# Optimization experiments

Hardware: AMD Instinct MI355X
Metric: run time of the kernel (lower is better)

Reference implementation:

```python
import jax, jax.numpy as jnp
import numpy as np

HIDDEN = 2048
N_HEADS = 32
N_KV = 8
HEAD_DIM = 64
B, S = 2, 2048
EPS = 1e-6
ROT_BASE = 10000.0


def _rms_norm(x, w):
    var = jnp.mean(x * x, axis=-1, keepdims=True)
    return x * jax.lax.rsqrt(var + EPS) * w


def _rotate_half(x):
    h = x.shape[-1] // 2
    return jnp.concatenate([-x[..., h:], x[..., :h]], axis=-1)


def _apply_rope(x, cos, sin):
    # x: [B,S,H,D], cos/sin: [S,D] -> broadcast over batch and heads
    c = cos[None, :, None, :]
    s = sin[None, :, None, :]
    return x * c + _rotate_half(x) * s


def setup_inputs() -> dict:
    key = jax.random.key(0)
    ks = jax.random.split(key, 12)
    sd = 0.02
    hidden_states = jax.random.normal(ks[0], (B, S, HIDDEN), dtype=jnp.float32)
    Wq = jax.random.normal(ks[1], (HIDDEN, N_HEADS * HEAD_DIM), dtype=jnp.float32) * sd
    bq = jnp.zeros((N_HEADS * HEAD_DIM,), dtype=jnp.float32)
    Wk = jax.random.normal(ks[2], (HIDDEN, N_KV * HEAD_DIM), dtype=jnp.float32) * sd
    bk = jnp.zeros((N_KV * HEAD_DIM,), dtype=jnp.float32)
    Wv = jax.random.normal(ks[3], (HIDDEN, N_KV * HEAD_DIM), dtype=jnp.float32) * sd
    bv = jnp.zeros((N_KV * HEAD_DIM,), dtype=jnp.float32)
    Wo = jax.random.normal(ks[4], (N_HEADS * HEAD_DIM, HIDDEN), dtype=jnp.float32) * sd
    bo = jnp.zeros((HIDDEN,), dtype=jnp.float32)
    qn_w = jnp.ones((HEAD_DIM,), dtype=jnp.float32)
    kn_w = jnp.ones((HEAD_DIM,), dtype=jnp.float32)
    # rotary tables (Llama convention: duplicated half-dim freqs)
    inv_freq = 1.0 / (ROT_BASE ** (np.arange(0, HEAD_DIM, 2, dtype=np.float32) / HEAD_DIM))
    t = np.arange(S, dtype=np.float32)
    freqs = np.outer(t, inv_freq)              # [S, D/2]
    emb = np.concatenate([freqs, freqs], axis=-1)  # [S, D]
    cos = jnp.asarray(np.cos(emb), dtype=jnp.float32)
    sin = jnp.asarray(np.sin(emb), dtype=jnp.float32)
    cu_seqlens = jnp.asarray([0, S, 2 * S], dtype=jnp.int32)
    return {"hidden_states": hidden_states, "Wq": Wq, "bq": bq, "Wk": Wk, "bk": bk,
            "Wv": Wv, "bv": bv, "Wo": Wo, "bo": bo, "qn_w": qn_w, "kn_w": kn_w,
            "cos": cos, "sin": sin, "cu_seqlens": cu_seqlens, "max_s": S}


def reference(hidden_states, Wq, bq, Wk, bk, Wv, bv, Wo, bo, qn_w, kn_w, cos, sin, cu_seqlens, max_s):
    b, s, _ = hidden_states.shape
    q = (hidden_states @ Wq + bq).reshape(b, s, N_HEADS, HEAD_DIM)
    k = (hidden_states @ Wk + bk).reshape(b, s, N_KV, HEAD_DIM)
    v = (hidden_states @ Wv + bv).reshape(b, s, N_KV, HEAD_DIM)
    q = _rms_norm(q, qn_w)
    k = _rms_norm(k, kn_w)
    q = _apply_rope(q, cos, sin)
    k = _apply_rope(k, cos, sin)
    # GQA: repeat_interleave kv heads to match query heads
    n_rep = N_HEADS // N_KV
    k = jnp.repeat(k, n_rep, axis=2)
    v = jnp.repeat(v, n_rep, axis=2)
    q = q.transpose(0, 2, 1, 3)  # [B,H,S,D]
    k = k.transpose(0, 2, 1, 3)
    v = v.transpose(0, 2, 1, 3)
    scale = 1.0 / jnp.sqrt(jnp.asarray(HEAD_DIM, dtype=q.dtype))
    scores = jnp.einsum("bhqd,bhkd->bhqk", q, k) * scale
    neg = jnp.finfo(scores.dtype).min
    causal = jnp.triu(jnp.ones((s, s), dtype=scores.dtype), k=1)  # [S,S]
    scores = scores + causal[None, None] * neg
    attn = jax.nn.softmax(scores, axis=-1)
    out = jnp.einsum("bhqk,bhkd->bhqd", attn, v)
    out = out.transpose(0, 2, 1, 3).reshape(b, s, N_HEADS * HEAD_DIM)
    return out @ Wo + bo
```

## Files before the change

### kernel.cpp

```cpp
#include <hip/hip_runtime.h>

typedef unsigned short u16;
typedef __attribute__((ext_vector_type(4))) float f32x4;
typedef __attribute__((ext_vector_type(16))) float f32x16;
typedef __attribute__((ext_vector_type(8))) short s16x8;
typedef __attribute__((ext_vector_type(8))) unsigned short u16x8;
typedef __attribute__((ext_vector_type(4))) unsigned short u16x4;

__device__ __forceinline__ float bf2f(u16 u) {
    union { unsigned int i; float f; } x; x.i = ((unsigned int)u) << 16; return x.f;
}
__device__ __forceinline__ u16 f2bf(float f) {
    union { float f; unsigned int i; } x; x.f = f;
    unsigned int r = x.i + 0x7FFFu + ((x.i >> 16) & 1u);
    return (u16)(r >> 16);
}
__device__ __forceinline__ void gload16(const void* g, void* l) {
    __builtin_amdgcn_global_load_lds((const __attribute__((address_space(1))) void*)g,
                                     (__attribute__((address_space(3))) void*)l, 16, 0, 0);
}
__device__ __forceinline__ unsigned cvtpk(float lo, float hi) {
    unsigned r;
    asm("v_cvt_pk_bf16_f32 %0, %1, %2" : "=v"(r) : "v"(lo), "v"(hi));
    return r;
}

#define BATCH 2
#define SEQ 2048
#define HID 2048
#define NH 32
#define NKV 8
#define HD 64
#define TOK (BATCH * SEQ)
#define NQKV 3072
#define QSCALE 0.18033688011112042f

__global__ void k_f32_to_bf16(const float* __restrict__ src, u16* __restrict__ dst, int n4) {
    int i = blockIdx.x * blockDim.x + threadIdx.x;
    if (i >= n4) return;
    f32x4 v = ((const f32x4*)src)[i];
    u16x4 o;
    o[0] = f2bf(v[0]); o[1] = f2bf(v[1]); o[2] = f2bf(v[2]); o[3] = f2bf(v[3]);
    *(u16x4*)(dst + (size_t)i * 4) = o;
}

__global__ void k_transpose_all(const float* __restrict__ Wq, const float* __restrict__ Wk,
                                const float* __restrict__ Wv, const float* __restrict__ Wo,
                                u16* __restrict__ WTqkv, u16* __restrict__ WoT) {
    __shared__ float tile[32][33];
    const int z = blockIdx.z;
    const float* src;
    u16* dst;
    int N;
    if (z == 0)      { src = Wq; dst = WTqkv;                              N = HID; }
    else if (z == 1) { src = Wk; dst = WTqkv + (size_t)HID * HID;          N = 512; }
    else if (z == 2) { src = Wv; dst = WTqkv + (size_t)(HID + 512) * HID;  N = 512; }
    else             { src = Wo; dst = WoT;                                N = HID; }
    int n0 = blockIdx.x * 32, k0 = blockIdx.y * 32;
    if (n0 >= N) return;
    int tx = threadIdx.x, ty = threadIdx.y;
#pragma unroll
    for (int i = 0; i < 4; i++)
        tile[ty + i * 8][tx] = src[(size_t)(k0 + ty + i * 8) * N + n0 + tx];
    __syncthreads();
#pragma unroll
    for (int i = 0; i < 4; i++) {
        int n = n0 + ty + i * 8;
        dst[(size_t)n * HID + k0 + tx] = f2bf(tile[tx][ty + i * 8]);
    }
}

__global__ void k_transpose_v(const u16* __restrict__ src, u16* __restrict__ dst) {
    __shared__ u16 tile[32][34];
    const u16* s = src + (size_t)blockIdx.z * SEQ * HD;
    u16* d = dst + (size_t)blockIdx.z * SEQ * HD;
    int d0 = blockIdx.x * 32;
    int s0 = blockIdx.y * 32;
    int tx = threadIdx.x, ty = threadIdx.y;
#pragma unroll
    for (int i = 0; i < 4; i++)
        tile[ty + i * 8][tx] = s[(size_t)(s0 + ty + i * 8) * HD + d0 + tx];
    __syncthreads();
#pragma unroll
    for (int i = 0; i < 4; i++)
        d[(size_t)(d0 + ty + i * 8) * SEQ + s0 + tx] = tile[tx][ty + i * 8];
}

__global__ __launch_bounds__(512, 1) void k_gemm256_qkv(const u16* __restrict__ A, const u16* __restrict__ BT,
                                                        const float* __restrict__ bq, const float* __restrict__ bk,
                                                        const float* __restrict__ bv,
                                                        const float* __restrict__ qn_w, const float* __restrict__ kn_w,
                                                        const float* __restrict__ cosT, const float* __restrict__ sinT,
                                                        u16* __restrict__ Qp, u16* __restrict__ Kp, u16* __restrict__ Vp,
                                                        int gxn, int K, int lda, int ldb) {
    __shared__ u16 LDS[2][2][256 * 64];
    const int tid = threadIdx.x;
    const int w = tid >> 6, lane = tid & 63;
    const int wm = w >> 2, wn = w & 3;
    const int lr = lane & 15, g = lane >> 4;
    const int nwg = gridDim.x;
    int bid = blockIdx.x;
    const int cpx = nwg >> 3;
    bid = (bid & 7) * cpx + (bid >> 3);
    const int brow = (bid / gxn) * 256, bcol = (bid % gxn) * 256;

    const int lrow8 = lane >> 3;
    const int gs = (lane & 7) ^ lrow8;
    const u16* Ag[4]; const u16* Bg[4];
#pragma unroll
    for (int p = 0; p < 4; p++) {
        int row = (w * 4 + p) * 8 + lrow8;
        Ag[p] = A + (size_t)(brow + row) * lda + gs * 8;
        Bg[p] = BT + (size_t)(bcol + row) * ldb + gs * 8;
    }

    f32x4 acc[8][4] = {};

#pragma unroll
    for (int p = 0; p < 4; p++) {
        gload16(Ag[p], &LDS[0][0][(w * 4 + p) * 512]);
        gload16(Bg[p], &LDS[0][1][(w * 4 + p) * 512]);
    }
    asm volatile("s_waitcnt vmcnt(0)" ::: "memory");
    __builtin_amdgcn_s_barrier();
    asm volatile("" ::: "memory");

    const int NT = K >> 6;
    int cur = 0;
    for (int tk = 0; tk < NT; tk++) {
        const u16* Al = &LDS[cur][0][0];
        const u16* Bl = &LDS[cur][1][0];
        u16* An = &LDS[cur ^ 1][0][0];
        u16* Bn = &LDS[cur ^ 1][1][0];
        const int knext = (tk + 1) << 6;
        const bool pf = (tk + 1 < NT);
        s16x8 bfr[4][2];
#pragma unroll
        for (int p = 0; p < 4; p++) {
            s16x8 af[2][2];
#pragma unroll
            for (int j = 0; j < 2; j++) {
                const char* rowp = (const char*)Al + (size_t)(wm * 128 + (2 * p + j) * 16 + lr) * 128;
#pragma unroll
                for (int kk = 0; kk < 2; kk++)
                    af[j][kk] = *(const s16x8*)(rowp + (((kk * 4 + g) ^ (lr & 7)) << 4));
            }
            if (p == 0) {
#pragma unroll
                for (int ni = 0; ni < 4; ni++) {
                    const char* rowp = (const char*)Bl + (size_t)(wn * 64 + ni * 16 + lr) * 128;
#pragma unroll
                    for (int kk = 0; kk < 2; kk++)
                        bfr[ni][kk] = *(const s16x8*)(rowp + (((kk * 4 + g) ^ (lr & 7)) << 4));
                }
            }
            if (pf) {
                gload16(Ag[p] + knext, &An[(w * 4 + p) * 512]);
                gload16(Bg[p] + knext, &Bn[(w * 4 + p) * 512]);
            }
            __builtin_amdgcn_s_barrier();
            __builtin_amdgcn_s_setprio(1);
#pragma unroll
            for (int j = 0; j < 2; j++)
#pragma unroll
                for (int ni = 0; ni < 4; ni++) {
                    acc[2 * p + j][ni] = __builtin_amdgcn_mfma_f32_16x16x32_bf16(af[j][0], bfr[ni][0], acc[2 * p + j][ni], 0, 0, 0);
                    acc[2 * p + j][ni] = __builtin_amdgcn_mfma_f32_16x16x32_bf16(af[j][1], bfr[ni][1], acc[2 * p + j][ni], 0, 0, 0);
                }
            __builtin_amdgcn_s_setprio(0);
            __builtin_amdgcn_s_barrier();
        }
        if (pf) asm volatile("s_waitcnt vmcnt(0)" ::: "memory");
        __builtin_amdgcn_s_barrier();
        asm volatile("" ::: "memory");
        cur ^= 1;
    }

    const int head = (bcol >> 6) + wn;
    const float* bptr = (head < 32) ? (bq + head * 64)
                       : (head < 40) ? (bk + (head - 32) * 64)
                                     : (bv + (head - 40) * 64);
    const float bz0 = bptr[0 * 16 + lr], bz1 = bptr[1 * 16 + lr];
    const float bz2 = bptr[2 * 16 + lr], bz3 = bptr[3 * 16 + lr];
    const float nw0 = (head < 32) ? qn_w[0 * 16 + lr] : kn_w[0 * 16 + lr];
    const float nw1 = (head < 32) ? qn_w[1 * 16 + lr] : kn_w[1 * 16 + lr];
    const float nw2 = (head < 32) ? qn_w[2 * 16 + lr] : kn_w[2 * 16 + lr];
    const float nw3 = (head < 32) ? qn_w[3 * 16 + lr] : kn_w[3 * 16 + lr];
#pragma unroll
    for (int mi = 0; mi < 8; mi++) {
#pragma unroll
        for (int r = 0; r < 4; r++) {
            int row = brow + wm * 128 + mi * 16 + g * 4 + r;
            int b = row >> 11, s = row & 2047;
            float v[4];
            v[0] = acc[mi][0][r] + bz0;
            v[1] = acc[mi][1][r] + bz1;
            v[2] = acc[mi][2][r] + bz2;
            v[3] = acc[mi][3][r] + bz3;
            if (head < 40) {
                float ss = v[0] * v[0] + v[1] * v[1] + v[2] * v[2] + v[3] * v[3];
                ss += __shfl_xor(ss, 1);
                ss += __shfl_xor(ss, 2);
                ss += __shfl_xor(ss, 4);
                ss += __shfl_xor(ss, 8);
                float rin = rsqrtf(ss * (1.0f / 64.0f) + 1e-6f);
                float xn[4];
                xn[0] = v[0] * rin * nw0;
                xn[1] = v[1] * rin * nw1;
                xn[2] = v[2] * rin * nw2;
                xn[3] = v[3] * rin * nw3;
                const float* cr = cosT + (size_t)s * HD;
                const float* sr = sinT + (size_t)s * HD;
                float o[4];
#pragma unroll
                for (int ni = 0; ni < 4; ni++) {
                    int d = ni * 16 + lr;
                    float part = xn[ni ^ 2];
                    float sign = (d < 32) ? -1.f : 1.f;
                    o[ni] = xn[ni] * cr[d] + sign * part * sr[d];
                }
                if (head < 32) {
                    u16* qrow = Qp + (((size_t)(b * NH + head) * SEQ + s) * HD);
#pragma unroll
                    for (int ni = 0; ni < 4; ni++) qrow[ni * 16 + lr] = f2bf(o[ni] * QSCALE);
                } else {
                    u16* krow = Kp + (((size_t)(b * NKV + head - 32) * SEQ + s) * HD);
#pragma unroll
                    for (int ni = 0; ni < 4; ni++) krow[ni * 16 + lr] = f2bf(o[ni]);
                }
            } else {
                u16* vrow = Vp + (((size_t)(b * NKV + head - 40) * SEQ + s) * HD);
#pragma unroll
                for (int ni = 0; ni < 4; ni++) vrow[ni * 16 + lr] = f2bf(v[ni]);
            }
        }
    }
}

__global__ __launch_bounds__(512, 1) void k_gemm_wo(const u16* __restrict__ A, const u16* __restrict__ BT,
                                                    const float* __restrict__ bias, float* __restrict__ Cout,
                                                    int gxn, int K, int lda, int ldb, int N) {
    __shared__ u16 LA[2][128 * 64];
    __shared__ u16 LB[2][256 * 64];
    const int tid = threadIdx.x;
    const int w = tid >> 6, lane = tid & 63;
    const int wm = w >> 2, wn = w & 3;
    const int lr = lane & 15, g = lane >> 4;
    const int nwg = gridDim.x;
    int bid = blockIdx.x;
    const int cpx = nwg >> 3;
    bid = (bid & 7) * cpx + (bid >> 3);
    const int brow = (bid / gxn) * 128, bcol = (bid % gxn) * 256;

    const int lrow8 = lane >> 3;
    const int gs = (lane & 7) ^ lrow8;
    const u16* Ag[2]; const u16* Bg[4];
#pragma unroll
    for (int p = 0; p < 2; p++) {
        int row = (w * 2 + p) * 8 + lrow8;
        Ag[p] = A + (size_t)(brow + row) * lda + gs * 8;
    }
#pragma unroll
    for (int p = 0; p < 4; p++) {
        int row = (w * 4 + p) * 8 + lrow8;
        Bg[p] = BT + (size_t)(bcol + row) * ldb + gs * 8;
    }

    f32x4 acc[4][4] = {};

#pragma unroll
    for (int p = 0; p < 2; p++) gload16(Ag[p], &LA[0][(w * 2 + p) * 512]);
#pragma unroll
    for (int p = 0; p < 4; p++) gload16(Bg[p], &LB[0][(w * 4 + p) * 512]);
    asm volatile("s_waitcnt vmcnt(0)" ::: "memory");
    __builtin_amdgcn_s_barrier();
    asm volatile("" ::: "memory");

    const int NT = K >> 6;
    int cur = 0;
    for (int tk = 0; tk < NT; tk++) {
        const u16* Al = &LA[cur][0];
        const u16* Bl = &LB[cur][0];
        u16* An = &LA[cur ^ 1][0];
        u16* Bn = &LB[cur ^ 1][0];
        const int knext = (tk + 1) << 6;
        const bool pf = (tk + 1 < NT);
        s16x8 bfr[4][2];
#pragma unroll
        for (int p = 0; p < 4; p++) {
            s16x8 af[2];
            const char* rowpA = (const char*)Al + (size_t)(wm * 64 + p * 16 + lr) * 128;
#pragma unroll
            for (int kk = 0; kk < 2; kk++)
                af[kk] = *(const s16x8*)(rowpA + (((kk * 4 + g) ^ (lr & 7)) << 4));
            if (p == 0) {
#pragma unroll
                for (int ni = 0; ni < 4; ni++) {
                    const char* rowp = (const char*)Bl + (size_t)(wn * 64 + ni * 16 + lr) * 128;
#pragma unroll
                    for (int kk = 0; kk < 2; kk++)
                        bfr[ni][kk] = *(const s16x8*)(rowp + (((kk * 4 + g) ^ (lr & 7)) << 4));
                }
            }
            if (pf) {
                if (p == 0) {
                    gload16(Ag[0] + knext, &An[(w * 2 + 0) * 512]);
                    gload16(Ag[1] + knext, &An[(w * 2 + 1) * 512]);
                } else if (p == 1) {
                    gload16(Bg[0] + knext, &Bn[(w * 4 + 0) * 512]);
                    gload16(Bg[1] + knext, &Bn[(w * 4 + 1) * 512]);
                } else if (p == 2) {
                    gload16(Bg[2] + knext, &Bn[(w * 4 + 2) * 512]);
                    gload16(Bg[3] + knext, &Bn[(w * 4 + 3) * 512]);
                }
            }
            __builtin_amdgcn_s_barrier();
            __builtin_amdgcn_s_setprio(1);
#pragma unroll
            for (int ni = 0; ni < 4; ni++) {
                acc[p][ni] = __builtin_amdgcn_mfma_f32_16x16x32_bf16(af[0], bfr[ni][0], acc[p][ni], 0, 0, 0);
                acc[p][ni] = __builtin_amdgcn_mfma_f32_16x16x32_bf16(af[1], bfr[ni][1], acc[p][ni], 0, 0, 0);
            }
            __builtin_amdgcn_s_setprio(0);
            __builtin_amdgcn_s_barrier();
        }
        if (pf) asm volatile("s_waitcnt vmcnt(0)" ::: "memory");
        __builtin_amdgcn_s_barrier();
        asm volatile("" ::: "memory");
        cur ^= 1;
    }

#pragma unroll
    for (int mi = 0; mi < 4; mi++) {
#pragma unroll
        for (int ni = 0; ni < 4; ni++) {
#pragma unroll
            for (int r = 0; r < 4; r++) {
                int row = brow + wm * 64 + mi * 16 + g * 4 + r;
                int col = bcol + wn * 64 + ni * 16 + lr;
                Cout[(size_t)row * N + col] = acc[mi][ni][r] + bias[col];
            }
        }
    }
}

__global__ __launch_bounds__(256) void k_attn_mfma(const u16* __restrict__ Qp, const u16* __restrict__ Kp,
                                                   const u16* __restrict__ VpT, u16* __restrict__ AO) {
    __shared__ u16 K_lds[64 * 64];
    __shared__ u16 VT_lds[64 * 64];
    __shared__ u16 P_lds[4][32][76];
    const int bid = blockIdx.x;
    const int qt = 15 - (bid >> 6);
    const int hh = bid & 63;
    const int b = hh >> 5, h = hh & 31, kvh = h >> 2;
    const int t = threadIdx.x, w = t >> 6, lane = t & 63;
    const int q5 = lane & 31, hi = lane >> 5;
    const int qwb = qt * 128 + w * 32;
    const int q_abs = qwb + q5;

    const u16* Qb = Qp + (size_t)(b * NH + h) * SEQ * HD;
    const u16* Kb = Kp + (size_t)(b * NKV + kvh) * SEQ * HD;
    const u16* Vb = VpT + (size_t)(b * NKV + kvh) * HD * SEQ;

    s16x8 qf0 = *(const s16x8*)(Qb + (size_t)q_abs * HD + 0 * 16 + hi * 8);
    s16x8 qf1 = *(const s16x8*)(Qb + (size_t)q_abs * HD + 1 * 16 + hi * 8);
    s16x8 qf2 = *(const s16x8*)(Qb + (size_t)q_abs * HD + 2 * 16 + hi * 8);
    s16x8 qf3 = *(const s16x8*)(Qb + (size_t)q_abs * HD + 3 * 16 + hi * 8);

    f32x16 O0, O1;
#pragma unroll
    for (int r = 0; r < 16; r++) { O0[r] = 0.f; O1[r] = 0.f; }
    float m = -1e30f, l = 0.f;

    const int swz = (q5 & 7) << 4;
    const int nkt = 2 * (qt + 1);
    for (int kt = 0; kt < nkt; kt++) {
        const int k0 = kt * 64;
        __syncthreads();
#pragma unroll
        for (int i = 0; i < 2; i++) {
            int c = (w * 2 + i) * 64 + lane;
            int row = c >> 3, gslot = (c & 7) ^ (row & 7);
            gload16(Kb + (size_t)(k0 + row) * HD + gslot * 8, (char*)K_lds + (size_t)(w * 2 + i) * 1024);
            gload16(Vb + (size_t)row * SEQ + k0 + gslot * 8, (char*)VT_lds + (size_t)(w * 2 + i) * 1024);
        }
        __syncthreads();
        if (k0 > qwb + 31) continue;

        f32x16 s0, s1;
#pragma unroll
        for (int r = 0; r < 16; r++) { s0[r] = 0.f; s1[r] = 0.f; }
        __builtin_amdgcn_s_setprio(1);
#pragma unroll
        for (int dblk = 0; dblk < 4; dblk++) {
            s16x8 kf0 = *(const s16x8*)((const char*)K_lds + q5 * 128 + ((dblk * 32 + hi * 16) ^ swz));
            s16x8 kf1 = *(const s16x8*)((const char*)K_lds + (32 + q5) * 128 + ((dblk * 32 + hi * 16) ^ swz));
            s16x8 qq = (dblk == 0) ? qf0 : (dblk == 1) ? qf1 : (dblk == 2) ? qf2 : qf3;
            s0 = __builtin_amdgcn_mfma_f32_32x32x16_bf16(kf0, qq, s0, 0, 0, 0);
            s1 = __builtin_amdgcn_mfma_f32_32x32x16_bf16(kf1, qq, s1, 0, 0, 0);
        }
        __builtin_amdgcn_s_setprio(0);

        if (k0 + 63 > qwb) {
            const int qrel = q_abs - k0;
#pragma unroll
            for (int r = 0; r < 16; r++) {
                int kr = (r & 3) + 8 * (r >> 2) + 4 * hi;
                if (kr > qrel) s0[r] = -1e30f;
                if (kr + 32 > qrel) s1[r] = -1e30f;
            }
        }

        float mt = -1e30f;
#pragma unroll
        for (int r = 0; r < 16; r++) { mt = fmaxf(mt, s0[r]); mt = fmaxf(mt, s1[r]); }
        mt = fmaxf(mt, __shfl_xor(mt, 32));
        if (!__all(mt <= m + 8.0f)) {
            float mn = fmaxf(m, mt);
            float f = exp2f(m - mn);
            l *= f;
#pragma unroll
            for (int r = 0; r < 16; r++) { O0[r] *= f; O1[r] *= f; }
            m = mn;
        }
        float ps = 0.f;
#pragma unroll
        for (int r = 0; r < 16; r++) {
            float p0 = exp2f(s0[r] - m);
            float p1 = exp2f(s1[r] - m);
            s0[r] = p0; s1[r] = p1;
            ps += p0 + p1;
        }
        ps += __shfl_xor(ps, 32);
        l += ps;

#pragma unroll
        for (int i = 0; i < 8; i++) {
            int key = 2 * (i & 1) + 8 * (i >> 1) + 4 * hi;
            *(unsigned*)&P_lds[w][q5][key]      = cvtpk(s0[2 * i], s0[2 * i + 1]);
            *(unsigned*)&P_lds[w][q5][key + 32] = cvtpk(s1[2 * i], s1[2 * i + 1]);
        }

        __builtin_amdgcn_s_setprio(1);
#pragma unroll
        for (int ks = 0; ks < 4; ks++) {
            s16x8 pb  = *(const s16x8*)&P_lds[w][q5][ks * 16 + hi * 8];
            s16x8 vf0 = *(const s16x8*)((const char*)VT_lds + q5 * 128 + ((ks * 32 + hi * 16) ^ swz));
            s16x8 vf1 = *(const s16x8*)((const char*)VT_lds + (32 + q5) * 128 + ((ks * 32 + hi * 16) ^ swz));
            O0 = __builtin_amdgcn_mfma_f32_32x32x16_bf16(vf0, pb, O0, 0, 0, 0);
            O1 = __builtin_amdgcn_mfma_f32_32x32x16_bf16(vf1, pb, O1, 0, 0, 0);
        }
        __builtin_amdgcn_s_setprio(0);
    }

    float inv = 1.0f / l;
    u16* orow = AO + (size_t)(b * SEQ + q_abs) * (NH * HD) + h * HD;
#pragma unroll
    for (int db = 0; db < 2; db++) {
#pragma unroll
        for (int g2 = 0; g2 < 4; g2++) {
            u16x4 wv;
#pragma unroll
            for (int i2 = 0; i2 < 4; i2++) {
                float v = (db == 0 ? O0[g2 * 4 + i2] : O1[g2 * 4 + i2]) * inv;
                wv[i2] = f2bf(v);
            }
            *(u16x4*)(orow + db * 32 + g2 * 8 + hi * 4) = wv;
        }
    }
}

extern "C" void kernel_launch(void* const* d_in, const int* in_sizes, int n_in,
                              void* d_out, int out_size, void* d_ws, size_t ws_size,
                              hipStream_t stream) {
    const float* hs   = (const float*)d_in[0];
    const float* Wq   = (const float*)d_in[1];
    const float* bq   = (const float*)d_in[2];
    const float* Wk   = (const float*)d_in[3];
    const float* bk   = (const float*)d_in[4];
    const float* Wv   = (const float*)d_in[5];
    const float* bv   = (const float*)d_in[6];
    const float* Wo   = (const float*)d_in[7];
    const float* bo   = (const float*)d_in[8];
    const float* qn_w = (const float*)d_in[9];
    const float* kn_w = (const float*)d_in[10];
    const float* cosT = (const float*)d_in[11];
    const float* sinT = (const float*)d_in[12];

    char* ws = (char*)d_ws;
    size_t off = 0;
    auto alloc = [&](size_t bytes) { char* p = ws + off; off = (off + bytes + 255) & ~(size_t)255; return p; };
    u16*   Xb    = (u16*)  alloc((size_t)TOK * HID * 2);
    u16*   WTqkv = (u16*)  alloc((size_t)NQKV * HID * 2);
    u16*   WoT   = (u16*)  alloc((size_t)HID * HID * 2);
    u16*   Qp    = (u16*)  alloc((size_t)BATCH * NH * SEQ * HD * 2);
    u16*   Kp    = (u16*)  alloc((size_t)BATCH * NKV * SEQ * HD * 2);
    u16*   Vp    = (u16*)  alloc((size_t)BATCH * NKV * SEQ * HD * 2);
    u16*   VpT   = (u16*)  alloc((size_t)BATCH * NKV * SEQ * HD * 2);
    u16*   AO    = (u16*)  alloc((size_t)TOK * HID * 2);
    (void)ws_size;

    k_f32_to_bf16<<<(TOK * HID / 4 + 255) / 256, 256, 0, stream>>>(hs, Xb, TOK * HID / 4);
    dim3 tb(32, 8);
    k_transpose_all<<<dim3(64, 64, 4), tb, 0, stream>>>(Wq, Wk, Wv, Wo, WTqkv, WoT);
    k_gemm256_qkv<<<dim3((TOK / 256) * (NQKV / 256)), 512, 0, stream>>>(
        Xb, WTqkv, bq, bk, bv, qn_w, kn_w, cosT, sinT, Qp, Kp, Vp, NQKV / 256, HID, HID, HID);
    k_transpose_v<<<dim3(HD / 32, SEQ / 32, BATCH * NKV), tb, 0, stream>>>(Vp, VpT);
    k_attn_mfma<<<BATCH * NH * (SEQ / 128), 256, 0, stream>>>(Qp, Kp, VpT, AO);
    k_gemm_wo<<<dim3((TOK / 128) * (HID / 256)), 512, 0, stream>>>(AO, WoT, bo, (float*)d_out,
                                                                    HID / 256, HID, HID, HID, HID);
}
```

Baseline: 229.3 us.

## Double-buffer K/V tiles in attention kernel to overlap loads with compute

Doubles the LDS buffers for K and V^T and prefetches the next 64-key tile via global_load_lds while the current tile is consumed. Explicit vmcnt waits and s_barrier replace the two __syncthreads per iteration, so the global-to-LDS latency can be hidden behind the MFMA and softmax work. This doubles the K/V LDS footprint, which may reduce occupancy. It also relies on hand-placed waitcnt and barriers being correct.

```diff
diff --git a/kernel.cpp b/kernel.cpp
--- a/kernel.cpp
+++ b/kernel.cpp
@@ -346,8 +346,8 @@
 
 __global__ __launch_bounds__(256) void k_attn_mfma(const u16* __restrict__ Qp, const u16* __restrict__ Kp,
                                                    const u16* __restrict__ VpT, u16* __restrict__ AO) {
-    __shared__ u16 K_lds[64 * 64];
-    __shared__ u16 VT_lds[64 * 64];
+    __shared__ u16 K_lds[2][64 * 64];
+    __shared__ u16 VT_lds[2][64 * 64];
     __shared__ u16 P_lds[4][32][76];
     const int bid = blockIdx.x;
     const int qt = 15 - (bid >> 6);
@@ -362,6 +362,10 @@
     const u16* Kb = Kp + (size_t)(b * NKV + kvh) * SEQ * HD;
     const u16* Vb = VpT + (size_t)(b * NKV + kvh) * HD * SEQ;
 
+    const int c0 = (w * 2 + 0) * 64 + lane, c1 = (w * 2 + 1) * 64 + lane;
+    const int r0 = c0 >> 3, g0 = (c0 & 7) ^ (r0 & 7);
+    const int r1 = c1 >> 3, g1 = (c1 & 7) ^ (r1 & 7);
+
     s16x8 qf0 = *(const s16x8*)(Qb + (size_t)q_abs * HD + 0 * 16 + hi * 8);
     s16x8 qf1 = *(const s16x8*)(Qb + (size_t)q_abs * HD + 1 * 16 + hi * 8);
     s16x8 qf2 = *(const s16x8*)(Qb + (size_t)q_abs * HD + 2 * 16 + hi * 8);
@@ -374,83 +378,103 @@
 
     const int swz = (q5 & 7) << 4;
     const int nkt = 2 * (qt + 1);
+
+    gload16(Kb + (size_t)r0 * HD + g0 * 8, (char*)K_lds[0] + (size_t)(w * 2 + 0) * 1024);
+    gload16(Kb + (size_t)r1 * HD + g1 * 8, (char*)K_lds[0] + (size_t)(w * 2 + 1) * 1024);
+    gload16(Vb + (size_t)r0 * SEQ + g0 * 8, (char*)VT_lds[0] + (size_t)(w * 2 + 0) * 1024);
+    gload16(Vb + (size_t)r1 * SEQ + g1 * 8, (char*)VT_lds[0] + (size_t)(w * 2 + 1) * 1024);
+    asm volatile("s_waitcnt vmcnt(0)" ::: "memory");
+    __builtin_amdgcn_s_barrier();
+    asm volatile("" ::: "memory");
+
     for (int kt = 0; kt < nkt; kt++) {
         const int k0 = kt * 64;
-        __syncthreads();
-#pragma unroll
-        for (int i = 0; i < 2; i++) {
-            int c = (w * 2 + i) * 64 + lane;
-            int row = c >> 3, gslot = (c & 7) ^ (row & 7);
-            gload16(Kb + (size_t)(k0 + row) * HD + gslot * 8, (char*)K_lds + (size_t)(w * 2 + i) * 1024);
-            gload16(Vb + (size_t)row * SEQ + k0 + gslot * 8, (char*)VT_lds + (size_t)(w * 2 + i) * 1024);
-        }
-        __syncthreads();
-        if (k0 > qwb + 31) continue;
-
-        f32x16 s0, s1;
-#pragma unroll
-        for (int r = 0; r < 16; r++) { s0[r] = 0.f; s1[r] = 0.f; }
-        __builtin_amdgcn_s_setprio(1);
-#pragma unroll
-        for (int dblk = 0; dblk < 4; dblk++) {
-            s16x8 kf0 = *(const s16x8*)((const char*)K_lds + q5 * 128 + ((dblk * 32 + hi * 16) ^ swz));
-            s16x8 kf1 = *(const s16x8*)((const char*)K_lds + (32 + q5) * 128 + ((dblk * 32 + hi * 16) ^ swz));
-            s16x8 qq = (dblk == 0) ? qf0 : (dblk == 1) ? qf1 : (dblk == 2) ? qf2 : qf3;
-            s0 = __builtin_amdgcn_mfma_f32_32x32x16_bf16(kf0, qq, s0, 0, 0, 0);
-            s1 = __builtin_amdgcn_mfma_f32_32x32x16_bf16(kf1, qq, s1, 0, 0, 0);
-        }
-        __builtin_amdgcn_s_setprio(0);
-
-        if (k0 + 63 > qwb) {
-            const int qrel = q_abs - k0;
+        const int cur = kt & 1;
+        if (kt + 1 < nkt) {
+            const int nk0 = k0 + 64;
+            gload16(Kb + (size_t)(nk0 + r0) * HD + g0 * 8, (char*)K_lds[cur ^ 1] + (size_t)(w * 2 + 0) * 1024);
+            gload16(Kb + (size_t)(nk0 + r1) * HD + g1 * 8, (char*)K_lds[cur ^ 1] + (size_t)(w * 2 + 1) * 1024);
+            gload16(Vb + (size_t)r0 * SEQ + nk0 + g0 * 8, (char*)VT_lds[cur ^ 1] + (size_t)(w * 2 + 0) * 1024);
+            gload16(Vb + (size_t)r1 * SEQ + nk0 + g1 * 8, (char*)VT_lds[cur ^ 1] + (size_t)(w * 2 + 1) * 1024);
+            asm volatile("s_waitcnt vmcnt(4)" ::: "memory");
+        } else {
+            asm volatile("s_waitcnt vmcnt(0)" ::: "memory");
+        }
+        __builtin_amdgcn_s_barrier();
+        asm volatile("" ::: "memory");
+
+        if (k0 <= qwb + 31) {
+            const char* Kc = (const char*)K_lds[cur];
+            const char* Vc = (const char*)VT_lds[cur];
+
+            f32x16 s0, s1;
+#pragma unroll
+            for (int r = 0; r < 16; r++) { s0[r] = 0.f; s1[r] = 0.f; }
+            __builtin_amdgcn_s_setprio(1);
+#pragma unroll
+            for (int dblk = 0; dblk < 4; dblk++) {
+                s16x8 kf0 = *(const s16x8*)(Kc + q5 * 128 + ((dblk * 32 + hi * 16) ^ swz));
+                s16x8 kf1 = *(const s16x8*)(Kc + (32 + q5) * 128 + ((dblk * 32 + hi * 16) ^ swz));
+                s16x8 qq = (dblk == 0) ? qf0 : (dblk == 1) ? qf1 : (dblk == 2) ? qf2 : qf3;
+                s0 = __builtin_amdgcn_mfma_f32_32x32x16_bf16(kf0, qq, s0, 0, 0, 0);
+                s1 = __builtin_amdgcn_mfma_f32_32x32x16_bf16(kf1, qq, s1, 0, 0, 0);
+            }
+            __builtin_amdgcn_s_setprio(0);
+
+            if (k0 + 63 > qwb) {
+                const int qrel = q_abs - k0;
+#pragma unroll
+                for (int r = 0; r < 16; r++) {
+                    int kr = (r & 3) + 8 * (r >> 2) + 4 * hi;
+                    if (kr > qrel) s0[r] = -1e30f;
+                    if (kr + 32 > qrel) s1[r] = -1e30f;
+                }
+            }
+
+            float mt = -1e30f;
+#pragma unroll
+            for (int r = 0; r < 16; r++) { mt = fmaxf(mt, s0[r]); mt = fmaxf(mt, s1[r]); }
+            mt = fmaxf(mt, __shfl_xor(mt, 32));
+            if (!__all(mt <= m + 8.0f)) {
+                float mn = fmaxf(m, mt);
+                float f = exp2f(m - mn);
+                l *= f;
+#pragma unroll
+                for (int r = 0; r < 16; r++) { O0[r] *= f; O1[r] *= f; }
+                m = mn;
+            }
+            float ps = 0.f;
 #pragma unroll
             for (int r = 0; r < 16; r++) {
-                int kr = (r & 3) + 8 * (r >> 2) + 4 * hi;
-                if (kr > qrel) s0[r] = -1e30f;
-                if (kr + 32 > qrel) s1[r] = -1e30f;
-            }
-        }
-
-        float mt = -1e30f;
-#pragma unroll
-        for (int r = 0; r < 16; r++) { mt = fmaxf(mt, s0[r]); mt = fmaxf(mt, s1[r]); }
-        mt = fmaxf(mt, __shfl_xor(mt, 32));
-        if (!__all(mt <= m + 8.0f)) {
-            float mn = fmaxf(m, mt);
-            float f = exp2f(m - mn);
-            l *= f;
-#pragma unroll
-            for (int r = 0; r < 16; r++) { O0[r] *= f; O1[r] *= f; }
-            m = mn;
-        }
-        float ps = 0.f;
-#pragma unroll
-        for (int r = 0; r < 16; r++) {
-            float p0 = exp2f(s0[r] - m);
-            float p1 = exp2f(s1[r] - m);
-            s0[r] = p0; s1[r] = p1;
-            ps += p0 + p1;
-        }
-        ps += __shfl_xor(ps, 32);
-        l += ps;
-
-#pragma unroll
-        for (int i = 0; i < 8; i++) {
-            int key = 2 * (i & 1) + 8 * (i >> 1) + 4 * hi;
-            *(unsigned*)&P_lds[w][q5][key]      = cvtpk(s0[2 * i], s0[2 * i + 1]);
-            *(unsigned*)&P_lds[w][q5][key + 32] = cvtpk(s1[2 * i], s1[2 * i + 1]);
-        }
-
-        __builtin_amdgcn_s_setprio(1);
-#pragma unroll
-        for (int ks = 0; ks < 4; ks++) {
-            s16x8 pb  = *(const s16x8*)&P_lds[w][q5][ks * 16 + hi * 8];
-            s16x8 vf0 = *(const s16x8*)((const char*)VT_lds + q5 * 128 + ((ks * 32 + hi * 16) ^ swz));
-            s16x8 vf1 = *(const s16x8*)((const char*)VT_lds + (32 + q5) * 128 + ((ks * 32 + hi * 16) ^ swz));
-            O0 = __builtin_amdgcn_mfma_f32_32x32x16_bf16(vf0, pb, O0, 0, 0, 0);
-            O1 = __builtin_amdgcn_mfma_f32_32x32x16_bf16(vf1, pb, O1, 0, 0, 0);
-        }
-        __builtin_amdgcn_s_setprio(0);
+                float p0 = exp2f(s0[r] - m);
+                float p1 = exp2f(s1[r] - m);
+                s0[r] = p0; s1[r] = p1;
+                ps += p0 + p1;
+            }
+            ps += __shfl_xor(ps, 32);
+            l += ps;
+
+#pragma unroll
+            for (int i = 0; i < 8; i++) {
+                int key = 2 * (i & 1) + 8 * (i >> 1) + 4 * hi;
+                *(unsigned*)&P_lds[w][q5][key]      = cvtpk(s0[2 * i], s0[2 * i + 1]);
+                *(unsigned*)&P_lds[w][q5][key + 32] = cvtpk(s1[2 * i], s1[2 * i + 1]);
+            }
+
+            __builtin_amdgcn_s_setprio(1);
+#pragma unroll
+            for (int ks = 0; ks < 4; ks++) {
+                s16x8 pb  = *(const s16x8*)&P_lds[w][q5][ks * 16 + hi * 8];
+                s16x8 vf0 = *(const s16x8*)(Vc + q5 * 128 + ((ks * 32 + hi * 16) ^ swz));
+                s16x8 vf1 = *(const s16x8*)(Vc + (32 + q5) * 128 + ((ks * 32 + hi * 16) ^ swz));
+                O0 = __builtin_amdgcn_mfma_f32_32x32x16_bf16(vf0, pb, O0, 0, 0, 0);
+                O1 = __builtin_amdgcn_mfma_f32_32x32x16_bf16(vf1, pb, O1, 0, 0, 0);
+            }
+            __builtin_amdgcn_s_setprio(0);
+        }
+
+        __builtin_amdgcn_s_barrier();
+        asm volatile("" ::: "memory");
     }
 
     float inv = 1.0f / l;
```

New measurement: 232.2 us. No clear change (+1.3%).

## Retile QKV GEMM to 256x192 with six waves and fuse input cast into prep

Applied to the files above, without the earlier changes.

The QKV projection GEMM goes from 256x256 tiles with 8 waves to 256x192 tiles with 6 waves (2x3 wave grid). That makes the grid 256 workgroups instead of 192, so it fills all 256 compute units in a single wave of tiles. Next-tile prefetch is now issued all at once at the first sub-step instead of spread over four sub-steps. Separately, the hidden-state f32-to-bf16 cast becomes an extra z-slice of the weight transpose kernel, which removes one launch. Risks: 192-column tiles straddle the Q/K projection boundary at column 2048, which the epilogue must handle, and the bunched prefetch may contend with the LDS reads.

```diff
diff --git a/kernel.cpp b/kernel.cpp
--- a/kernel.cpp
+++ b/kernel.cpp
@@ -35,20 +35,24 @@
 #define NQKV 3072
 #define QSCALE 0.18033688011112042f
 
-__global__ void k_f32_to_bf16(const float* __restrict__ src, u16* __restrict__ dst, int n4) {
-    int i = blockIdx.x * blockDim.x + threadIdx.x;
-    if (i >= n4) return;
-    f32x4 v = ((const f32x4*)src)[i];
-    u16x4 o;
-    o[0] = f2bf(v[0]); o[1] = f2bf(v[1]); o[2] = f2bf(v[2]); o[3] = f2bf(v[3]);
-    *(u16x4*)(dst + (size_t)i * 4) = o;
-}
-
-__global__ void k_transpose_all(const float* __restrict__ Wq, const float* __restrict__ Wk,
-                                const float* __restrict__ Wv, const float* __restrict__ Wo,
-                                u16* __restrict__ WTqkv, u16* __restrict__ WoT) {
+__global__ void k_prep(const float* __restrict__ Wq, const float* __restrict__ Wk,
+                       const float* __restrict__ Wv, const float* __restrict__ Wo,
+                       const float* __restrict__ hs,
+                       u16* __restrict__ WTqkv, u16* __restrict__ WoT, u16* __restrict__ Xb) {
     __shared__ float tile[32][33];
     const int z = blockIdx.z;
+    int tx = threadIdx.x, ty = threadIdx.y;
+    if (z == 4) {
+        int blk = blockIdx.y * 64 + blockIdx.x;
+        size_t base = ((size_t)blk * 256 + (ty * 32 + tx)) * 8;
+        f32x4 v0 = *(const f32x4*)(hs + base);
+        f32x4 v1 = *(const f32x4*)(hs + base + 4);
+        u16x8 o;
+        o[0] = f2bf(v0[0]); o[1] = f2bf(v0[1]); o[2] = f2bf(v0[2]); o[3] = f2bf(v0[3]);
+        o[4] = f2bf(v1[0]); o[5] = f2bf(v1[1]); o[6] = f2bf(v1[2]); o[7] = f2bf(v1[3]);
+        *(u16x8*)(Xb + base) = o;
+        return;
+    }
     const float* src;
     u16* dst;
     int N;
@@ -58,7 +62,6 @@
     else             { src = Wo; dst = WoT;                                N = HID; }
     int n0 = blockIdx.x * 32, k0 = blockIdx.y * 32;
     if (n0 >= N) return;
-    int tx = threadIdx.x, ty = threadIdx.y;
 #pragma unroll
     for (int i = 0; i < 4; i++)
         tile[ty + i * 8][tx] = src[(size_t)(k0 + ty + i * 8) * N + n0 + tx];
@@ -86,41 +89,35 @@
         d[(size_t)(d0 + ty + i * 8) * SEQ + s0 + tx] = tile[tx][ty + i * 8];
 }
 
-__global__ __launch_bounds__(512, 1) void k_gemm256_qkv(const u16* __restrict__ A, const u16* __restrict__ BT,
+__global__ __launch_bounds__(384, 1) void k_gemm_qkv192(const u16* __restrict__ A, const u16* __restrict__ BT,
                                                         const float* __restrict__ bq, const float* __restrict__ bk,
                                                         const float* __restrict__ bv,
                                                         const float* __restrict__ qn_w, const float* __restrict__ kn_w,
                                                         const float* __restrict__ cosT, const float* __restrict__ sinT,
                                                         u16* __restrict__ Qp, u16* __restrict__ Kp, u16* __restrict__ Vp,
-                                                        int gxn, int K, int lda, int ldb) {
-    __shared__ u16 LDS[2][2][256 * 64];
+                                                        int K, int lda, int ldb) {
+    __shared__ u16 LA[2][256 * 64];
+    __shared__ u16 LB[2][192 * 64];
     const int tid = threadIdx.x;
     const int w = tid >> 6, lane = tid & 63;
-    const int wm = w >> 2, wn = w & 3;
+    const int wm = w / 3, wn = w % 3;
     const int lr = lane & 15, g = lane >> 4;
     const int nwg = gridDim.x;
     int bid = blockIdx.x;
     const int cpx = nwg >> 3;
     bid = (bid & 7) * cpx + (bid >> 3);
-    const int brow = (bid / gxn) * 256, bcol = (bid % gxn) * 256;
+    const int gxn = NQKV / 192;
+    const int brow = (bid / gxn) * 256, bcol = (bid % gxn) * 192;
 
     const int lrow8 = lane >> 3;
     const int gs = (lane & 7) ^ lrow8;
-    const u16* Ag[4]; const u16* Bg[4];
-#pragma unroll
-    for (int p = 0; p < 4; p++) {
-        int row = (w * 4 + p) * 8 + lrow8;
-        Ag[p] = A + (size_t)(brow + row) * lda + gs * 8;
-        Bg[p] = BT + (size_t)(bcol + row) * ldb + gs * 8;
-    }
 
     f32x4 acc[8][4] = {};
 
-#pragma unroll
-    for (int p = 0; p < 4; p++) {
-        gload16(Ag[p], &LDS[0][0][(w * 4 + p) * 512]);
-        gload16(Bg[p], &LDS[0][1][(w * 4 + p) * 512]);
-    }
+    for (int c = w; c < 32; c += 6)
+        gload16(A + (size_t)(brow + c * 8 + lrow8) * lda + gs * 8, &LA[0][c * 512]);
+    for (int c = w; c < 24; c += 6)
+        gload16(BT + (size_t)(bcol + c * 8 + lrow8) * ldb + gs * 8, &LB[0][c * 512]);
     asm volatile("s_waitcnt vmcnt(0)" ::: "memory");
     __builtin_amdgcn_s_barrier();
     asm volatile("" ::: "memory");
@@ -128,10 +125,10 @@
     const int NT = K >> 6;
     int cur = 0;
     for (int tk = 0; tk < NT; tk++) {
-        const u16* Al = &LDS[cur][0][0];
-        const u16* Bl = &LDS[cur][1][0];
-        u16* An = &LDS[cur ^ 1][0][0];
-        u16* Bn = &LDS[cur ^ 1][1][0];
+        const u16* Al = &LA[cur][0];
+        const u16* Bl = &LB[cur][0];
+        u16* An = &LA[cur ^ 1][0];
+        u16* Bn = &LB[cur ^ 1][0];
         const int knext = (tk + 1) << 6;
         const bool pf = (tk + 1 < NT);
         s16x8 bfr[4][2];
@@ -153,10 +150,12 @@
                     for (int kk = 0; kk < 2; kk++)
                         bfr[ni][kk] = *(const s16x8*)(rowp + (((kk * 4 + g) ^ (lr & 7)) << 4));
                 }
-            }
-            if (pf) {
-                gload16(Ag[p] + knext, &An[(w * 4 + p) * 512]);
-                gload16(Bg[p] + knext, &Bn[(w * 4 + p) * 512]);
+                if (pf) {
+                    for (int c = w; c < 32; c += 6)
+                        gload16(A + (size_t)(brow + c * 8 + lrow8) * lda + knext + gs * 8, &An[c * 512]);
+                    for (int c = w; c < 24; c += 6)
+                        gload16(BT + (size_t)(bcol + c * 8 + lrow8) * ldb + knext + gs * 8, &Bn[c * 512]);
+                }
             }
             __builtin_amdgcn_s_barrier();
             __builtin_amdgcn_s_setprio(1);
@@ -500,11 +499,10 @@
     u16*   AO    = (u16*)  alloc((size_t)TOK * HID * 2);
     (void)ws_size;
 
-    k_f32_to_bf16<<<(TOK * HID / 4 + 255) / 256, 256, 0, stream>>>(hs, Xb, TOK * HID / 4);
     dim3 tb(32, 8);
-    k_transpose_all<<<dim3(64, 64, 4), tb, 0, stream>>>(Wq, Wk, Wv, Wo, WTqkv, WoT);
-    k_gemm256_qkv<<<dim3((TOK / 256) * (NQKV / 256)), 512, 0, stream>>>(
-        Xb, WTqkv, bq, bk, bv, qn_w, kn_w, cosT, sinT, Qp, Kp, Vp, NQKV / 256, HID, HID, HID);
+    k_prep<<<dim3(64, 64, 5), tb, 0, stream>>>(Wq, Wk, Wv, Wo, hs, WTqkv, WoT, Xb);
+    k_gemm_qkv192<<<dim3(16 * 16), 384, 0, stream>>>(
+        Xb, WTqkv, bq, bk, bv, qn_w, kn_w, cosT, sinT, Qp, Kp, Vp, HID, HID, HID);
     k_transpose_v<<<dim3(HD / 32, SEQ / 32, BATCH * NKV), tb, 0, stream>>>(Vp, VpT);
     k_attn_mfma<<<BATCH * NH * (SEQ / 128), 256, 0, stream>>>(Qp, Kp, VpT, AO);
     k_gemm_wo<<<dim3((TOK / 128) * (HID / 256)), 512, 0, stream>>>(AO, WoT, bo, (float*)d_out,
```

Result: no change. 231.7 us (+1.0%).
